# Optimization experiments

Hardware: AMD Instinct MI355X
Metric: run time of the kernel (lower is better)

Reference implementation:

```python
import jax, jax.numpy as jnp
import numpy as np

EMBED = 1024
HEADS = 16
HEAD_DIM = EMBED // HEADS


def setup_inputs() -> dict:
    key = jax.random.key(0)
    ks = jax.random.split(key, 8)
    N, L = 4, 2048
    inp = {
        "values": jax.random.normal(ks[0], (N, L, EMBED), dtype=jnp.float32),
        "keys": jax.random.normal(ks[1], (N, L, EMBED), dtype=jnp.float32),
        "query": jax.random.normal(ks[2], (N, L, EMBED), dtype=jnp.float32),
        # per-head-dim projections (torch Linear: y = x @ W.T), no bias
        "Wv": jax.random.normal(ks[3], (HEAD_DIM, HEAD_DIM), dtype=jnp.float32) * (1.0 / np.sqrt(HEAD_DIM)),
        "Wk": jax.random.normal(ks[4], (HEAD_DIM, HEAD_DIM), dtype=jnp.float32) * (1.0 / np.sqrt(HEAD_DIM)),
        "Wq": jax.random.normal(ks[5], (HEAD_DIM, HEAD_DIM), dtype=jnp.float32) * (1.0 / np.sqrt(HEAD_DIM)),
        # output projection with bias
        "Wo": jax.random.normal(ks[6], (EMBED, EMBED), dtype=jnp.float32) * (1.0 / np.sqrt(EMBED)),
        "bo": jax.random.normal(ks[7], (EMBED,), dtype=jnp.float32) * 0.01,
    }
    return inp


def reference(values, keys, query, Wv, Wk, Wq, Wo, bo):
    N, Lq, _ = query.shape
    Lv = values.shape[1]
    Lk = keys.shape[1]
    # split heads: [N, L, H, D]
    v = values.reshape(N, Lv, HEADS, HEAD_DIM)
    k = keys.reshape(N, Lk, HEADS, HEAD_DIM)
    q = query.reshape(N, Lq, HEADS, HEAD_DIM)
    # per-head-dim linear projections (x @ W.T)
    v = jnp.einsum("nlhd,ed->nlhe", v, Wv)
    k = jnp.einsum("nlhd,ed->nlhe", k, Wk)
    q = jnp.einsum("nlhd,ed->nlhe", q, Wq)
    # scores: [N, H, Q, K]; note scale is sqrt(embed_size), matching source
    energy = jnp.einsum("nqhd,nkhd->nhqk", q, k)
    attention = jax.nn.softmax(energy / jnp.sqrt(jnp.float32(EMBED)), axis=-1)
    # weighted values: [N, Q, H, D] -> [N, Q, E]
    out = jnp.einsum("nhql,nlhd->nqhd", attention, v).reshape(N, Lq, EMBED)
    # output projection
    return out @ Wo.T + bo
```

## Files before the change

kernel.cpp:

```cpp
#include <hip/hip_runtime.h>
#include <hip/hip_bf16.h>

typedef __bf16 bf16;
typedef __bf16 bf16x2 __attribute__((ext_vector_type(2)));
typedef __bf16 bf16x4 __attribute__((ext_vector_type(4)));
typedef __bf16 bf16x8 __attribute__((ext_vector_type(8)));
typedef float f32x4 __attribute__((ext_vector_type(4)));

#define MFMA16(a, b, c) __builtin_amdgcn_mfma_f32_16x16x32_bf16((a), (b), (c), 0, 0, 0)

#if __has_builtin(__builtin_amdgcn_exp2f)
#define EXP2(x) __builtin_amdgcn_exp2f(x)
#else
#define EXP2(x) exp2f(x)
#endif

constexpr int EMBED = 1024;
constexpr int HEADS = 16;
constexpr int HD = 64;
constexpr int SEQ = 2048;
constexpr int LDSP = 72;
constexpr int SXTP = 76;
constexpr int WO_N = EMBED * EMBED;

#define QSCALE 0.04508422082f

static __device__ __forceinline__ unsigned pack2(float a, float b) {
    bf16x2 t;
    t[0] = (bf16)a;
    t[1] = (bf16)b;
    return __builtin_bit_cast(unsigned, t);
}
#define SWAP32(x, y) asm("v_permlane32_swap_b32 %0, %1" : "+v"(x), "+v"(y))
#define SWAP16(x, y) asm("v_permlane16_swap_b32 %0, %1" : "+v"(x), "+v"(y))

__global__ __launch_bounds__(256) void convert_weights(
    const float* __restrict__ Wo, const float* __restrict__ Wq,
    const float* __restrict__ Wk, const float* __restrict__ Wv,
    bf16* __restrict__ Wob, bf16* __restrict__ Wqb,
    bf16* __restrict__ Wkb, bf16* __restrict__ Wvb) {
    int gid = blockIdx.x * 256 + threadIdx.x;
    int base = gid * 8;
    const float* src;
    bf16* dst;
    float sc = 1.0f;
    int off;
    if (base < WO_N) {
        src = Wo; dst = Wob; off = base;
    } else {
        int j = base - WO_N;
        int w = j >> 12;
        off = j & 4095;
        src = (w == 0) ? Wq : (w == 1) ? Wk : Wv;
        dst = (w == 0) ? Wqb : (w == 1) ? Wkb : Wvb;
        if (w == 0) sc = QSCALE;
    }
    float4 a = *(const float4*)(src + off);
    float4 b = *(const float4*)(src + off + 4);
    bf16x8 o;
    o[0] = (bf16)(a.x * sc); o[1] = (bf16)(a.y * sc);
    o[2] = (bf16)(a.z * sc); o[3] = (bf16)(a.w * sc);
    o[4] = (bf16)(b.x * sc); o[5] = (bf16)(b.y * sc);
    o[6] = (bf16)(b.z * sc); o[7] = (bf16)(b.w * sc);
    *(bf16x8*)(dst + off) = o;
}

__global__ __launch_bounds__(256) void proj_kernel(
    const float* __restrict__ Vx, const float* __restrict__ Kx, const float* __restrict__ Qx,
    const bf16* __restrict__ Wqb, const bf16* __restrict__ Wkb, const bf16* __restrict__ Wvb,
    bf16* __restrict__ Vt, bf16* __restrict__ Kp, bf16* __restrict__ Qp) {
    __shared__ __align__(16) bf16 sT0[64 * LDSP];
    __shared__ __align__(16) bf16 sT1[64 * LDSP];
    __shared__ __align__(16) bf16 sXT[64 * SXTP];
    int g = blockIdx.x;
    int bid = (g & 7) * 256 + (g >> 3);
    int t = threadIdx.x, lane = t & 63, wq = t >> 6;
    int m = lane & 15, q8 = lane >> 4;
    int rowbase = bid * 64;
    int Arow = rowbase + wq * 16 + m;
    const float* Xs[3] = {Qx, Kx, Vx};
    const bf16* Ws[3] = {Wqb, Wkb, Wvb};
    f32x4 z = {0.f, 0.f, 0.f, 0.f};

    float4 ax[3][2][2];
#pragma unroll
    for (int ts = 0; ts < 3; ts++)
#pragma unroll
        for (int c = 0; c < 2; c++) {
            const float* s = Xs[ts] + (size_t)Arow * 64 + c * 32 + q8 * 8;
            ax[ts][c][0] = *(const float4*)s;
            ax[ts][c][1] = *(const float4*)(s + 4);
        }

#pragma unroll
    for (int ts = 0; ts < 3; ts++) {
        bf16x8 af[2];
#pragma unroll
        for (int c = 0; c < 2; c++) {
            float4 x0 = ax[ts][c][0];
            float4 x1 = ax[ts][c][1];
            bf16x8 a;
            a[0] = (bf16)x0.x; a[1] = (bf16)x0.y; a[2] = (bf16)x0.z; a[3] = (bf16)x0.w;
            a[4] = (bf16)x1.x; a[5] = (bf16)x1.y; a[6] = (bf16)x1.z; a[7] = (bf16)x1.w;
            af[c] = a;
        }
        bf16x8 bfr[4][2];
#pragma unroll
        for (int nt = 0; nt < 4; nt++)
#pragma unroll
            for (int c = 0; c < 2; c++)
                bfr[nt][c] = *(const bf16x8*)(Ws[ts] + (nt * 16 + m) * 64 + c * 32 + q8 * 8);
        f32x4 acc[4] = {z, z, z, z};
#pragma unroll
        for (int c = 0; c < 2; c++)
#pragma unroll
            for (int nt = 0; nt < 4; nt++)
                acc[nt] = MFMA16(af[c], bfr[nt][c], acc[nt]);

        if (ts < 2) {
            bf16* sT = (ts == 0) ? sT0 : sT1;
            for (int nt = 0; nt < 4; nt++)
                for (int jr = 0; jr < 4; jr++)
                    sT[(wq * 16 + q8 * 4 + jr) * LDSP + nt * 16 + m] = (bf16)acc[nt][jr];
            __syncthreads();
            int r = t >> 2, c4 = t & 3;
            int R = rowbase + r;
            int h = R & 15, l = (R >> 4) & 2047, n = R >> 15;
            bf16* dst = ((ts == 0) ? Qp : Kp) + ((size_t)(n * HEADS + h) * SEQ + l) * HD + c4 * 16;
            bf16x8 v0 = *(const bf16x8*)&sT[r * LDSP + c4 * 16];
            bf16x8 v1 = *(const bf16x8*)&sT[r * LDSP + c4 * 16 + 8];
            *(bf16x8*)dst = v0;
            *(bf16x8*)(dst + 8) = v1;
        } else {
            for (int nt = 0; nt < 4; nt++) {
                bf16x4 pv;
                pv[0] = (bf16)acc[nt][0]; pv[1] = (bf16)acc[nt][1];
                pv[2] = (bf16)acc[nt][2]; pv[3] = (bf16)acc[nt][3];
                *(bf16x4*)&sXT[(nt * 16 + m) * SXTP + wq * 16 + q8 * 4] = pv;
            }
            __syncthreads();
            int n = rowbase >> 15, l0 = (rowbase >> 4) & 2047;
            for (int i = t; i < 1024; i += 256) {
                int e = i & 63, hh = i >> 6;
                bf16x4 pv;
                pv[0] = sXT[e * SXTP + 0 * 16 + hh];
                pv[1] = sXT[e * SXTP + 1 * 16 + hh];
                pv[2] = sXT[e * SXTP + 2 * 16 + hh];
                pv[3] = sXT[e * SXTP + 3 * 16 + hh];
                *(bf16x4*)(Vt + ((size_t)(n * HEADS + hh) * HD + e) * SEQ + l0) = pv;
            }
        }
    }
}

__global__ __launch_bounds__(256, 2) void flash_kernel(
    const bf16* __restrict__ Qp, const bf16* __restrict__ Kp, const bf16* __restrict__ Vt,
    bf16* __restrict__ O) {
    int nh = blockIdx.x, qt = blockIdx.y;
    int n = nh >> 4, h = nh & 15;
    int t = threadIdx.x, lane = t & 63, wq = t >> 6;
    int m = lane & 15, q8 = lane >> 4;
    __shared__ __align__(16) bf16 sK[2 * 64 * LDSP];
    __shared__ __align__(16) bf16 sV[2 * 64 * LDSP];
    size_t nhs = (size_t)nh;
    int qb = qt * 256 + wq * 64;
    const bf16* Qb = Qp + (nhs * SEQ + qb) * HD;
    const bf16* Kb = Kp + nhs * SEQ * HD;
    const bf16* Vb = Vt + nhs * (size_t)HD * SEQ;

    bool isK = t < 128;
    int t2 = isK ? t : t - 128;
    int srow = t2 >> 1, shalf = t2 & 1;
    const bf16* sbase = isK ? (Kb + (size_t)srow * HD + shalf * 32)
                            : (Vb + (size_t)srow * SEQ + shalf * 32);
    size_t sstride = isK ? (size_t)HD : 1;
    bf16* ldst0 = (isK ? sK : sV) + srow * LDSP + shalf * 32;

    bf16x8 qf[4][2];
    for (int ntq = 0; ntq < 4; ntq++)
        for (int c = 0; c < 2; c++)
            qf[ntq][c] = *(const bf16x8*)(Qb + (ntq * 16 + m) * HD + c * 32 + q8 * 8);

    bf16x8 ones;
    for (int i = 0; i < 8; i++) ones[i] = (bf16)1.0f;

    f32x4 z = {0.f, 0.f, 0.f, 0.f};
    f32x4 accO[4][4];
    for (int a = 0; a < 4; a++)
        for (int b = 0; b < 4; b++) accO[a][b] = z;
    f32x4 accL[4] = {z, z, z, z};

    bf16x8 stg[4];
    auto load_stage = [&](int kb) {
#pragma unroll
        for (int j = 0; j < 4; j++)
            stg[j] = *(const bf16x8*)(sbase + (size_t)kb * sstride + j * 8);
    };
    auto write_stage = [&](int p) {
        bf16* d = ldst0 + p * (64 * LDSP);
#pragma unroll
        for (int j = 0; j < 4; j++)
            *(bf16x8*)(d + j * 8) = stg[j];
    };

    load_stage(0);
    write_stage(0);
    __syncthreads();
    load_stage(64);

    int p = 0;
    for (int kb = 0; kb < SEQ; kb += 64) {
        const bf16* kB = sK + p * (64 * LDSP);
        const bf16* vB = sV + p * (64 * LDSP);
        bf16x8 kf[4][2];
#pragma unroll
        for (int kt = 0; kt < 4; kt++)
#pragma unroll
            for (int c = 0; c < 2; c++)
                kf[kt][c] = *(const bf16x8*)&kB[(kt * 16 + m) * LDSP + c * 32 + q8 * 8];
        bf16x8 vf[4][2];
#pragma unroll
        for (int dt = 0; dt < 4; dt++)
#pragma unroll
            for (int c = 0; c < 2; c++)
                vf[dt][c] = *(const bf16x8*)&vB[(dt * 16 + m) * LDSP + c * 32 + q8 * 8];
        write_stage(p ^ 1);
        load_stage((kb + 128) & (SEQ - 1));

#pragma unroll
        for (int ntq = 0; ntq < 4; ntq++) {
            f32x4 st[4];
#pragma unroll
            for (int kt = 0; kt < 4; kt++) st[kt] = z;
#pragma unroll
            for (int c = 0; c < 2; c++)
#pragma unroll
                for (int kt = 0; kt < 4; kt++)
                    st[kt] = MFMA16(kf[kt][c], qf[ntq][c], st[kt]);
            f32x4 pr[4];
#pragma unroll
            for (int kt = 0; kt < 4; kt++) {
                pr[kt][0] = EXP2(st[kt][0]);
                pr[kt][1] = EXP2(st[kt][1]);
                pr[kt][2] = EXP2(st[kt][2]);
                pr[kt][3] = EXP2(st[kt][3]);
            }
            bf16x8 pf[2];
#pragma unroll
            for (int c = 0; c < 2; c++) {
                unsigned dw[4];
#pragma unroll
                for (int i = 0; i < 2; i++) {
                    unsigned u = pack2(pr[2 * c][2 * i], pr[2 * c][2 * i + 1]);
                    unsigned v = pack2(pr[2 * c + 1][2 * i], pr[2 * c + 1][2 * i + 1]);
                    SWAP32(u, v);
                    SWAP16(u, v);
                    dw[i] = u;
                    dw[2 + i] = v;
                }
                union { unsigned u[4]; bf16x8 v; } cvt;
                cvt.u[0] = dw[0]; cvt.u[1] = dw[1];
                cvt.u[2] = dw[2]; cvt.u[3] = dw[3];
                pf[c] = cvt.v;
            }
#pragma unroll
            for (int c = 0; c < 2; c++) {
#pragma unroll
                for (int dt = 0; dt < 4; dt++)
                    accO[ntq][dt] = MFMA16(pf[c], vf[dt][c], accO[ntq][dt]);
                accL[ntq] = MFMA16(pf[c], ones, accL[ntq]);
            }
        }
        __syncthreads();
        p ^= 1;
    }

    for (int mtq = 0; mtq < 4; mtq++)
        for (int j = 0; j < 4; j++) {
            float iv = 1.0f / accL[mtq][j];
            int q = qb + mtq * 16 + q8 * 4 + j;
            size_t ro = ((size_t)n * SEQ + q) * EMBED + h * HD;
            for (int dt = 0; dt < 4; dt++)
                O[ro + dt * 16 + m] = (bf16)(accO[mtq][dt][j] * iv);
        }
}

__global__ __launch_bounds__(256, 2) void outproj_kernel(
    const bf16* __restrict__ O, const bf16* __restrict__ Wob,
    const float* __restrict__ bo, float* __restrict__ out) {
    __shared__ __align__(16) bf16 sA[2 * 128 * LDSP];
    __shared__ __align__(16) bf16 sB[2 * 128 * LDSP];
    int bid = blockIdx.x;
    int xcd = bid & 7, idx = bid >> 3;
    int qt = xcd * 8 + (idx & 7), et = idx >> 3;
    int t = threadIdx.x, lane = t & 63, wq = t >> 6;
    int m = lane & 15, q8 = lane >> 4;
    int wr = wq >> 1, wc = wq & 1;
    int qb = qt * 128, cb = et * 128;

    bool isA = t < 128;
    int r = t & 127;
    const bf16* sbase = isA ? (O + (size_t)(qb + r) * EMBED)
                            : (Wob + (size_t)(cb + r) * EMBED);
    bf16* ldst0 = (isA ? sA : sB) + r * LDSP;

    bf16x8 stg[8];
    auto load_stage = [&](int kk) {
#pragma unroll
        for (int j = 0; j < 8; j++)
            stg[j] = *(const bf16x8*)(sbase + kk + j * 8);
    };
    auto write_stage = [&](int p) {
        bf16* d = ldst0 + p * (128 * LDSP);
#pragma unroll
        for (int j = 0; j < 8; j++)
            *(bf16x8*)(d + j * 8) = stg[j];
    };

    f32x4 z = {0.f, 0.f, 0.f, 0.f};
    f32x4 acc[4][4];
    for (int a = 0; a < 4; a++)
        for (int b = 0; b < 4; b++) acc[a][b] = z;

    load_stage(0);
    write_stage(0);
    __syncthreads();
    load_stage(64);

    int p = 0;
    for (int kk = 0; kk < EMBED; kk += 64) {
        const bf16* aB = sA + p * (128 * LDSP);
        const bf16* bB = sB + p * (128 * LDSP);
        bf16x8 af[4][2], bfr[4][2];
#pragma unroll
        for (int mt = 0; mt < 4; mt++)
#pragma unroll
            for (int c = 0; c < 2; c++)
                af[mt][c] = *(const bf16x8*)&aB[(wr * 64 + mt * 16 + m) * LDSP + c * 32 + q8 * 8];
#pragma unroll
        for (int nt = 0; nt < 4; nt++)
#pragma unroll
            for (int c = 0; c < 2; c++)
                bfr[nt][c] = *(const bf16x8*)&bB[(wc * 64 + nt * 16 + m) * LDSP + c * 32 + q8 * 8];
        write_stage(p ^ 1);
        load_stage((kk + 128) & (EMBED - 1));

#pragma unroll
        for (int c = 0; c < 2; c++)
#pragma unroll
            for (int mt = 0; mt < 4; mt++)
#pragma unroll
                for (int nt = 0; nt < 4; nt++)
                    acc[mt][nt] = MFMA16(af[mt][c], bfr[nt][c], acc[mt][nt]);
        __syncthreads();
        p ^= 1;
    }

    for (int nt = 0; nt < 4; nt++) {
        int col = cb + wc * 64 + nt * 16 + m;
        float bias = bo[col];
        for (int mt = 0; mt < 4; mt++)
            for (int j = 0; j < 4; j++) {
                int q = qb + wr * 64 + mt * 16 + q8 * 4 + j;
                out[(size_t)q * EMBED + col] = acc[mt][nt][j] + bias;
            }
    }
}

extern "C" void kernel_launch(void* const* d_in, const int* in_sizes, int n_in,
                              void* d_out, int out_size, void* d_ws, size_t ws_size,
                              hipStream_t stream) {
    const float* values = (const float*)d_in[0];
    const float* keys   = (const float*)d_in[1];
    const float* query  = (const float*)d_in[2];
    const float* Wv     = (const float*)d_in[3];
    const float* Wk     = (const float*)d_in[4];
    const float* Wq     = (const float*)d_in[5];
    const float* Wo     = (const float*)d_in[6];
    const float* bo     = (const float*)d_in[7];
    float* out = (float*)d_out;

    char* ws = (char*)d_ws;
    bf16* Qp  = (bf16*)(ws);
    bf16* Kp  = (bf16*)(ws + (size_t)(16 << 20));
    bf16* Vt  = (bf16*)(ws + (size_t)(32 << 20));
    bf16* O   = (bf16*)(ws + (size_t)(48 << 20));
    bf16* Wob = (bf16*)(ws + (size_t)(64 << 20));
    bf16* Wqb = (bf16*)(ws + (size_t)(66 << 20));
    bf16* Wkb = (bf16*)(ws + (size_t)(66 << 20) + 8192);
    bf16* Wvb = (bf16*)(ws + (size_t)(66 << 20) + 16384);

    hipLaunchKernelGGL(convert_weights, dim3(518), dim3(256), 0, stream,
                       Wo, Wq, Wk, Wv, Wob, Wqb, Wkb, Wvb);
    hipLaunchKernelGGL(proj_kernel, dim3(2048), dim3(256), 0, stream,
                       values, keys, query, Wqb, Wkb, Wvb, Vt, Kp, Qp);
    hipLaunchKernelGGL(flash_kernel, dim3(64, 8), dim3(256), 0, stream, Qp, Kp, Vt, O);
    hipLaunchKernelGGL(outproj_kernel, dim3(512), dim3(256), 0, stream, O, Wob, bo, out);
}
```

Measured before the change: 274.1 us.

## Shrink outproj tile to 64x128 with single-buffered LDS and more blocks

```diff
diff --git a/kernel.cpp b/kernel.cpp
--- a/kernel.cpp
+++ b/kernel.cpp
@@ -285,64 +285,70 @@
         }
 }
 
-__global__ __launch_bounds__(256, 2) void outproj_kernel(
+__global__ __launch_bounds__(256, 3) void outproj_kernel(
     const bf16* __restrict__ O, const bf16* __restrict__ Wob,
     const float* __restrict__ bo, float* __restrict__ out) {
-    __shared__ __align__(16) bf16 sA[2 * 128 * LDSP];
-    __shared__ __align__(16) bf16 sB[2 * 128 * LDSP];
+    __shared__ __align__(16) bf16 sA[64 * LDSP];
+    __shared__ __align__(16) bf16 sB[128 * LDSP];
     int bid = blockIdx.x;
     int xcd = bid & 7, idx = bid >> 3;
-    int qt = xcd * 8 + (idx & 7), et = idx >> 3;
+    int qt = xcd * 16 + (idx & 15), et = idx >> 4;
     int t = threadIdx.x, lane = t & 63, wq = t >> 6;
     int m = lane & 15, q8 = lane >> 4;
-    int wr = wq >> 1, wc = wq & 1;
-    int qb = qt * 128, cb = et * 128;
+    int qb = qt * 64, cb = et * 128;
 
     bool isA = t < 128;
-    int r = t & 127;
-    const bf16* sbase = isA ? (O + (size_t)(qb + r) * EMBED)
-                            : (Wob + (size_t)(cb + r) * EMBED);
-    bf16* ldst0 = (isA ? sA : sB) + r * LDSP;
+    int rA = t >> 1, hf = t & 1;
+    int rB = t - 128;
+    const bf16* sbase = isA ? (O + (size_t)(qb + rA) * EMBED + hf * 32)
+                            : (Wob + (size_t)(cb + rB) * EMBED);
+    bf16* ldst = isA ? (sA + rA * LDSP + hf * 32) : (sB + rB * LDSP);
 
     bf16x8 stg[8];
     auto load_stage = [&](int kk) {
-#pragma unroll
-        for (int j = 0; j < 8; j++)
-            stg[j] = *(const bf16x8*)(sbase + kk + j * 8);
+        if (isA) {
+#pragma unroll
+            for (int j = 0; j < 4; j++) stg[j] = *(const bf16x8*)(sbase + kk + j * 8);
+        } else {
+#pragma unroll
+            for (int j = 0; j < 8; j++) stg[j] = *(const bf16x8*)(sbase + kk + j * 8);
+        }
     };
-    auto write_stage = [&](int p) {
-        bf16* d = ldst0 + p * (128 * LDSP);
-#pragma unroll
-        for (int j = 0; j < 8; j++)
-            *(bf16x8*)(d + j * 8) = stg[j];
+    auto write_stage = [&]() {
+        if (isA) {
+#pragma unroll
+            for (int j = 0; j < 4; j++) *(bf16x8*)(ldst + j * 8) = stg[j];
+        } else {
+#pragma unroll
+            for (int j = 0; j < 8; j++) *(bf16x8*)(ldst + j * 8) = stg[j];
+        }
     };
 
     f32x4 z = {0.f, 0.f, 0.f, 0.f};
-    f32x4 acc[4][4];
+    f32x4 acc[4][2];
     for (int a = 0; a < 4; a++)
-        for (int b = 0; b < 4; b++) acc[a][b] = z;
+        for (int b = 0; b < 2; b++) acc[a][b] = z;
 
     load_stage(0);
-    write_stage(0);
+    write_stage();
     __syncthreads();
     load_stage(64);
 
-    int p = 0;
     for (int kk = 0; kk < EMBED; kk += 64) {
-        const bf16* aB = sA + p * (128 * LDSP);
-        const bf16* bB = sB + p * (128 * LDSP);
-        bf16x8 af[4][2], bfr[4][2];
+        bf16x8 af[4][2], bfr[2][2];
 #pragma unroll
         for (int mt = 0; mt < 4; mt++)
 #pragma unroll
             for (int c = 0; c < 2; c++)
-                af[mt][c] = *(const bf16x8*)&aB[(wr * 64 + mt * 16 + m) * LDSP + c * 32 + q8 * 8];
-#pragma unroll
-        for (int nt = 0; nt < 4; nt++)
-#pragma unroll
-            for (int c = 0; c < 2; c++)
-                bfr[nt][c] = *(const bf16x8*)&bB[(wc * 64 + nt * 16 + m) * LDSP + c * 32 + q8 * 8];
-        write_stage(p ^ 1);
+                af[mt][c] = *(const bf16x8*)&sA[(mt * 16 + m) * LDSP + c * 32 + q8 * 8];
+#pragma unroll
+        for (int nt = 0; nt < 2; nt++)
+#pragma unroll
+            for (int c = 0; c < 2; c++)
+                bfr[nt][c] = *(const bf16x8*)&sB[(wq * 32 + nt * 16 + m) * LDSP + c * 32 + q8 * 8];
+        __syncthreads();
+        write_stage();
+        __syncthreads();
         load_stage((kk + 128) & (EMBED - 1));
 
 #pragma unroll
@@ -350,18 +356,16 @@
 #pragma unroll
             for (int mt = 0; mt < 4; mt++)
 #pragma unroll
-                for (int nt = 0; nt < 4; nt++)
+                for (int nt = 0; nt < 2; nt++)
                     acc[mt][nt] = MFMA16(af[mt][c], bfr[nt][c], acc[mt][nt]);
-        __syncthreads();
-        p ^= 1;
     }
 
-    for (int nt = 0; nt < 4; nt++) {
-        int col = cb + wc * 64 + nt * 16 + m;
+    for (int nt = 0; nt < 2; nt++) {
+        int col = cb + wq * 32 + nt * 16 + m;
         float bias = bo[col];
         for (int mt = 0; mt < 4; mt++)
             for (int j = 0; j < 4; j++) {
-                int q = qb + wr * 64 + mt * 16 + q8 * 4 + j;
+                int q = qb + mt * 16 + q8 * 4 + j;
                 out[(size_t)q * EMBED + col] = acc[mt][nt][j] + bias;
             }
     }
@@ -395,5 +399,5 @@
     hipLaunchKernelGGL(proj_kernel, dim3(2048), dim3(256), 0, stream,
                        values, keys, query, Wqb, Wkb, Wvb, Vt, Kp, Qp);
     hipLaunchKernelGGL(flash_kernel, dim3(64, 8), dim3(256), 0, stream, Qp, Kp, Vt, O);
-    hipLaunchKernelGGL(outproj_kernel, dim3(512), dim3(256), 0, stream, O, Wob, bo, out);
-}
+    hipLaunchKernelGGL(outproj_kernel, dim3(1024), dim3(256), 0, stream, O, Wob, bo, out);
+}
```

Result: no change. 279.0 us (+1.8%).
